# Optimization experiments

Measured on AMD Instinct MI355X. Metric: run time of the kernel, lower is better.

Reference implementation:

```python
import jax, jax.numpy as jnp
import numpy as np

NODES = 14      # input_size: nodes per graph
IN_F = 24       # seq_len: node feature dim
HID1 = 32
HID2 = 64       # hid_feats
HEADS = 2
OUT = 24        # output_size
B = 2048        # number of graphs
SLOPE = 0.2


def _make_edges():
    # fully connected (no self loops) within each 14-node graph
    pairs = np.array([(i, j) for i in range(NODES) for j in range(NODES) if i != j]).T  # [2,182]
    offs = (np.arange(B) * NODES)[:, None]
    src = (pairs[0][None, :] + offs).reshape(-1)
    dst = (pairs[1][None, :] + offs).reshape(-1)
    return np.stack([src, dst]).astype(np.int32)  # [2, 372736]


def setup_inputs() -> dict:
    key = jax.random.key(0)
    ks = jax.random.split(key, 16)
    N = B * NODES
    x = jax.random.normal(ks[0], (N, IN_F), dtype=jnp.float32)
    y = jax.random.normal(ks[1], (N, OUT), dtype=jnp.float32)
    edge_index = jnp.asarray(_make_edges())
    batch = jnp.repeat(jnp.arange(B, dtype=jnp.int32), NODES)
    s = 0.1
    params = dict(
        W1=jax.random.normal(ks[2], (IN_F, HEADS * HID1), dtype=jnp.float32) * s,
        a_src1=jax.random.normal(ks[3], (HEADS, HID1), dtype=jnp.float32) * s,
        a_dst1=jax.random.normal(ks[4], (HEADS, HID1), dtype=jnp.float32) * s,
        b1=jnp.zeros((HID1,), dtype=jnp.float32),
        W2=jax.random.normal(ks[5], (HID1, HEADS * HID2), dtype=jnp.float32) * s,
        a_src2=jax.random.normal(ks[6], (HEADS, HID2), dtype=jnp.float32) * s,
        a_dst2=jax.random.normal(ks[7], (HEADS, HID2), dtype=jnp.float32) * s,
        b2=jnp.zeros((HID2,), dtype=jnp.float32),
        Wf1=jax.random.normal(ks[8], (NODES, HID2, 8), dtype=jnp.float32) * s,
        bf1=jnp.zeros((NODES, 8), dtype=jnp.float32),
        Wf2=jax.random.normal(ks[9], (NODES, 8, OUT), dtype=jnp.float32) * s,
        bf2=jnp.zeros((NODES, OUT), dtype=jnp.float32),
    )
    return {"x": x, "y": y, "edge_index": edge_index, "batch": batch, **params}


def gat_conv(x, src, dst, W, a_src, a_dst, b):
    # PyG GATConv, concat=False (mean over heads), self-loops already in src/dst
    N = x.shape[0]
    H, F = a_src.shape
    xh = (x @ W).reshape(N, H, F)                       # [N,H,F]
    al_s = (xh * a_src).sum(-1)                         # [N,H]
    al_d = (xh * a_dst).sum(-1)                         # [N,H]
    alpha = jax.nn.leaky_relu(al_s[src] + al_d[dst], SLOPE)  # [E,H]
    amax = jax.ops.segment_max(alpha, dst, num_segments=N)
    ex = jnp.exp(alpha - amax[dst])
    den = jax.ops.segment_sum(ex, dst, num_segments=N)
    w = ex / den[dst]                                   # softmax per target node
    out = jax.ops.segment_sum(w[:, :, None] * xh[src], dst, num_segments=N)  # [N,H,F]
    return out.mean(axis=1) + b


def reference(x, y, edge_index, batch, W1, a_src1, a_dst1, b1, W2, a_src2, a_dst2, b2, Wf1, bf1, Wf2, bf2):
    N = x.shape[0]
    loops = jnp.arange(N, dtype=edge_index.dtype)
    src = jnp.concatenate([edge_index[0], loops])
    dst = jnp.concatenate([edge_index[1], loops])
    h = jax.nn.elu(gat_conv(x, src, dst, W1, a_src1, a_dst1, b1))   # [N,32]
    h = gat_conv(h, src, dst, W2, a_src2, a_dst2, b2)               # [N,64]
    # batch regroup: batch ids are contiguous per graph, so the Python
    # gather-loop in the original is exactly a reshape
    nb = N // NODES
    xg = h.reshape(nb, NODES, HID2).transpose(1, 0, 2)   # [14, B, 64]
    yg = y.reshape(nb, NODES, OUT)                       # [B, 14, out]
    # per-node-index MLP ensemble, batched over the 14 indices
    hh = jax.nn.relu(jnp.einsum('kbh,kho->kbo', xg, Wf1) + bf1[:, None, :])
    pred = jax.nn.sigmoid(jnp.einsum('kbo,kop->kbp', hh, Wf2) + bf2[:, None, :])  # [14,B,out]
    return pred, yg
```

## Files before the change

### kernel.cpp

```cpp
#include <hip/hip_runtime.h>

#define NODES 14
#define IN_F 24
#define HID1 32
#define HID2 64
#define OUT_F 24
#define SLOPE 0.2f

#define U_US1 0
#define U_UD1 48
#define U_US2 96
#define U_UD2 160

#define GPB 4
#define H1_S 36
#define H2_S 68
#define WT_S 20
#define PHASE_FENCE() __builtin_amdgcn_sched_barrier(0)

__global__ __launch_bounds__(256) void compute_uvecs(
    const float* __restrict__ W1, const float* __restrict__ a_src1,
    const float* __restrict__ a_dst1,
    const float* __restrict__ W2, const float* __restrict__ a_src2,
    const float* __restrict__ a_dst2, float* __restrict__ u)
{
  const int tid = threadIdx.x;
  if (tid < 96) {
    const int sd = (tid >= 48), r = tid - sd * 48;
    const int h = (r >= IN_F), k = r - h * IN_F;
    const float* av = sd ? a_dst1 : a_src1;
    float s = 0.f;
#pragma unroll
    for (int f = 0; f < HID1; ++f)
      s += W1[k * 64 + h * HID1 + f] * av[h * HID1 + f];
    u[(sd ? U_UD1 : U_US1) + h * IN_F + k] = s;
  } else if (tid < 224) {
    const int j = tid - 96;
    const int sd = (j >= 64), r = j - sd * 64;
    const int h = (r >= HID1), k = r - h * HID1;
    const float* av = sd ? a_dst2 : a_src2;
    float s = 0.f;
#pragma unroll
    for (int f = 0; f < HID2; ++f)
      s += W2[k * 128 + h * HID2 + f] * av[h * HID2 + f];
    u[(sd ? U_UD2 : U_US2) + h * HID1 + k] = s;
  }
}

__global__ __launch_bounds__(64 * GPB) void gnn_fused(
    const float* __restrict__ x, const float* __restrict__ y,
    const float* __restrict__ W1, const float* __restrict__ b1,
    const float* __restrict__ W2, const float* __restrict__ b2,
    const float* __restrict__ Wf1, const float* __restrict__ bf1,
    const float* __restrict__ Wf2, const float* __restrict__ bf2,
    const float* __restrict__ uvec,
    float* __restrict__ out, int ngraphs)
{
  const int tid  = threadIdx.x;
  const int lane = tid & 63;
  const int wv   = tid >> 6;
  const int gu   = __builtin_amdgcn_readfirstlane(blockIdx.x * GPB + wv);
  if (gu >= ngraphs) return;

  __shared__ __align__(16) float h1s[GPB][NODES * H1_S];
  __shared__ __align__(16) float h2s[GPB][NODES * H2_S];
  __shared__ __align__(16) float wt[GPB][28 * WT_S];
  __shared__ __align__(16) float als[GPB][32];
  __shared__ __align__(16) float ald[GPB][32];
  __shared__ __align__(16) float hhs[GPB][112];

  const float* xg = x + (size_t)gu * (NODES * IN_F);

  float w1r[IN_F];
#pragma unroll
  for (int k = 0; k < IN_F; ++k) w1r[k] = W1[k * 64 + lane];
  float w2r[64];
#pragma unroll
  for (int k = 0; k < HID1; ++k) {
    w2r[k]      = W2[k * 128 + lane];
    w2r[32 + k] = W2[k * 128 + 64 + lane];
  }
  PHASE_FENCE();

  {
    const float4* y4 = (const float4*)(y + (size_t)gu * (NODES * OUT_F));
    float4* o4 = (float4*)(out + (size_t)NODES * ngraphs * OUT_F
                               + (size_t)gu * (NODES * OUT_F));
    for (int i = lane; i < (NODES * OUT_F) / 4; i += 64) o4[i] = y4[i];
  }

  float xcol[NODES];
#pragma unroll 2
  for (int n = 0; n < NODES; ++n) {
    float acc = 0.f;
#pragma unroll
    for (int k = 0; k < IN_F; ++k) acc += xg[n * IN_F + k] * w1r[k];
    xcol[n] = acc;
  }

  if (lane < 56) {
    const int n = lane >> 2, h = (lane >> 1) & 1, sd = lane & 1;
    const float* uu = uvec + (sd ? U_UD1 : U_US1) + h * IN_F;
    float s = 0.f;
#pragma unroll
    for (int k4 = 0; k4 < 6; ++k4) {
      const float4 xv = *(const float4*)&xg[n * IN_F + k4 * 4];
      const float4 uv = *(const float4*)&uu[k4 * 4];
      s += xv.x * uv.x + xv.y * uv.y + xv.z * uv.z + xv.w * uv.w;
    }
    (sd ? ald : als)[wv][h * 16 + n] = s;
  }
  if (lane < NODES * 2) {
    const int j = lane >> 1, h = lane & 1;
    const float ad = ald[wv][h * 16 + j];
    const float4 A0 = *(const float4*)&als[wv][h * 16 + 0];
    const float4 A1 = *(const float4*)&als[wv][h * 16 + 4];
    const float4 A2 = *(const float4*)&als[wv][h * 16 + 8];
    const float2 A3 = *(const float2*)&als[wv][h * 16 + 12];
    float a[NODES] = {A0.x, A0.y, A0.z, A0.w, A1.x, A1.y, A1.z, A1.w,
                      A2.x, A2.y, A2.z, A2.w, A3.x, A3.y};
    float m = -1e30f;
#pragma unroll
    for (int i = 0; i < NODES; ++i) {
      float v = a[i] + ad;
      v = v > 0.f ? v : SLOPE * v;
      a[i] = v; m = fmaxf(m, v);
    }
    float den = 0.f;
#pragma unroll
    for (int i = 0; i < NODES; ++i) { a[i] = __expf(a[i] - m); den += a[i]; }
    const float r = 1.f / den;
    float* wr = &wt[wv][(j * 2 + h) * WT_S];
    *(float4*)&wr[0]  = make_float4(a[0]*r,  a[1]*r,  a[2]*r,  a[3]*r);
    *(float4*)&wr[4]  = make_float4(a[4]*r,  a[5]*r,  a[6]*r,  a[7]*r);
    *(float4*)&wr[8]  = make_float4(a[8]*r,  a[9]*r,  a[10]*r, a[11]*r);
    *(float2*)&wr[12] = make_float2(a[12]*r, a[13]*r);
  }

  {
    const int h = lane >> 5, f5 = lane & 31;
    const float bb = b1[f5];
#pragma unroll 2
    for (int n = 0; n < NODES; ++n) {
      const float* wr = &wt[wv][(n * 2 + h) * WT_S];
      const float4 w0 = *(const float4*)&wr[0];
      const float4 w1 = *(const float4*)&wr[4];
      const float4 w2 = *(const float4*)&wr[8];
      const float2 w3 = *(const float2*)&wr[12];
      float o = w0.x*xcol[0] + w0.y*xcol[1] + w0.z*xcol[2] + w0.w*xcol[3]
              + w1.x*xcol[4] + w1.y*xcol[5] + w1.z*xcol[6] + w1.w*xcol[7]
              + w2.x*xcol[8] + w2.y*xcol[9] + w2.z*xcol[10] + w2.w*xcol[11]
              + w3.x*xcol[12] + w3.y*xcol[13];
      const float oo = __shfl_xor(o, 32);
      if (h == 0) {
        const float v = 0.5f * (o + oo) + bb;
        h1s[wv][n * H1_S + f5] = v > 0.f ? v : expm1f(v);
      }
    }
  }
  PHASE_FENCE();

  float acc0[NODES], acc1[NODES];
#pragma unroll 2
  for (int n = 0; n < NODES; ++n) {
    const float4 v0 = *(const float4*)&h1s[wv][n * H1_S + 0];
    const float4 v1 = *(const float4*)&h1s[wv][n * H1_S + 4];
    const float4 v2 = *(const float4*)&h1s[wv][n * H1_S + 8];
    const float4 v3 = *(const float4*)&h1s[wv][n * H1_S + 12];
    const float4 v4 = *(const float4*)&h1s[wv][n * H1_S + 16];
    const float4 v5 = *(const float4*)&h1s[wv][n * H1_S + 20];
    const float4 v6 = *(const float4*)&h1s[wv][n * H1_S + 24];
    const float4 v7 = *(const float4*)&h1s[wv][n * H1_S + 28];
    acc0[n] = v0.x*w2r[0] + v0.y*w2r[1] + v0.z*w2r[2] + v0.w*w2r[3]
            + v1.x*w2r[4] + v1.y*w2r[5] + v1.z*w2r[6] + v1.w*w2r[7]
            + v2.x*w2r[8] + v2.y*w2r[9] + v2.z*w2r[10] + v2.w*w2r[11]
            + v3.x*w2r[12] + v3.y*w2r[13] + v3.z*w2r[14] + v3.w*w2r[15]
            + v4.x*w2r[16] + v4.y*w2r[17] + v4.z*w2r[18] + v4.w*w2r[19]
            + v5.x*w2r[20] + v5.y*w2r[21] + v5.z*w2r[22] + v5.w*w2r[23]
            + v6.x*w2r[24] + v6.y*w2r[25] + v6.z*w2r[26] + v6.w*w2r[27]
            + v7.x*w2r[28] + v7.y*w2r[29] + v7.z*w2r[30] + v7.w*w2r[31];
    acc1[n] = v0.x*w2r[32] + v0.y*w2r[33] + v0.z*w2r[34] + v0.w*w2r[35]
            + v1.x*w2r[36] + v1.y*w2r[37] + v1.z*w2r[38] + v1.w*w2r[39]
            + v2.x*w2r[40] + v2.y*w2r[41] + v2.z*w2r[42] + v2.w*w2r[43]
            + v3.x*w2r[44] + v3.y*w2r[45] + v3.z*w2r[46] + v3.w*w2r[47]
            + v4.x*w2r[48] + v4.y*w2r[49] + v4.z*w2r[50] + v4.w*w2r[51]
            + v5.x*w2r[52] + v5.y*w2r[53] + v5.z*w2r[54] + v5.w*w2r[55]
            + v6.x*w2r[56] + v6.y*w2r[57] + v6.z*w2r[58] + v6.w*w2r[59]
            + v7.x*w2r[60] + v7.y*w2r[61] + v7.z*w2r[62] + v7.w*w2r[63];
  }

  if (lane < 56) {
    const int n = lane >> 2, h = (lane >> 1) & 1, sd = lane & 1;
    const float* uu = uvec + (sd ? U_UD2 : U_US2) + h * HID1;
    float s = 0.f;
#pragma unroll
    for (int k4 = 0; k4 < 8; ++k4) {
      const float4 hv = *(const float4*)&h1s[wv][n * H1_S + k4 * 4];
      const float4 uv = *(const float4*)&uu[k4 * 4];
      s += hv.x * uv.x + hv.y * uv.y + hv.z * uv.z + hv.w * uv.w;
    }
    (sd ? ald : als)[wv][h * 16 + n] = s;
  }
  if (lane < NODES * 2) {
    const int j = lane >> 1, h = lane & 1;
    const float ad = ald[wv][h * 16 + j];
    const float4 A0 = *(const float4*)&als[wv][h * 16 + 0];
    const float4 A1 = *(const float4*)&als[wv][h * 16 + 4];
    const float4 A2 = *(const float4*)&als[wv][h * 16 + 8];
    const float2 A3 = *(const float2*)&als[wv][h * 16 + 12];
    float a[NODES] = {A0.x, A0.y, A0.z, A0.w, A1.x, A1.y, A1.z, A1.w,
                      A2.x, A2.y, A2.z, A2.w, A3.x, A3.y};
    float m = -1e30f;
#pragma unroll
    for (int i = 0; i < NODES; ++i) {
      float v = a[i] + ad;
      v = v > 0.f ? v : SLOPE * v;
      a[i] = v; m = fmaxf(m, v);
    }
    float den = 0.f;
#pragma unroll
    for (int i = 0; i < NODES; ++i) { a[i] = __expf(a[i] - m); den += a[i]; }
    const float r = 1.f / den;
    float* wr = &wt[wv][(j * 2 + h) * WT_S];
    *(float4*)&wr[0]  = make_float4(a[0]*r,  a[1]*r,  a[2]*r,  a[3]*r);
    *(float4*)&wr[4]  = make_float4(a[4]*r,  a[5]*r,  a[6]*r,  a[7]*r);
    *(float4*)&wr[8]  = make_float4(a[8]*r,  a[9]*r,  a[10]*r, a[11]*r);
    *(float2*)&wr[12] = make_float2(a[12]*r, a[13]*r);
  }

  {
    const float bb = b2[lane];
#pragma unroll 2
    for (int n = 0; n < NODES; ++n) {
      const float* wr0 = &wt[wv][(n * 2 + 0) * WT_S];
      const float* wr1 = &wt[wv][(n * 2 + 1) * WT_S];
      const float4 p0 = *(const float4*)&wr0[0];
      const float4 p1 = *(const float4*)&wr0[4];
      const float4 p2 = *(const float4*)&wr0[8];
      const float2 p3 = *(const float2*)&wr0[12];
      const float4 q0 = *(const float4*)&wr1[0];
      const float4 q1 = *(const float4*)&wr1[4];
      const float4 q2 = *(const float4*)&wr1[8];
      const float2 q3 = *(const float2*)&wr1[12];
      const float o0 = p0.x*acc0[0] + p0.y*acc0[1] + p0.z*acc0[2] + p0.w*acc0[3]
                     + p1.x*acc0[4] + p1.y*acc0[5] + p1.z*acc0[6] + p1.w*acc0[7]
                     + p2.x*acc0[8] + p2.y*acc0[9] + p2.z*acc0[10] + p2.w*acc0[11]
                     + p3.x*acc0[12] + p3.y*acc0[13];
      const float o1 = q0.x*acc1[0] + q0.y*acc1[1] + q0.z*acc1[2] + q0.w*acc1[3]
                     + q1.x*acc1[4] + q1.y*acc1[5] + q1.z*acc1[6] + q1.w*acc1[7]
                     + q2.x*acc1[8] + q2.y*acc1[9] + q2.z*acc1[10] + q2.w*acc1[11]
                     + q3.x*acc1[12] + q3.y*acc1[13];
      h2s[wv][n * H2_S + lane] = 0.5f * (o0 + o1) + bb;
    }
  }
  PHASE_FENCE();

  for (int idx = lane; idx < NODES * 8; idx += 64) {
    const int k = idx >> 3, e = idx & 7;
    float acc = bf1[k * 8 + e];
#pragma unroll
    for (int f4 = 0; f4 < 16; ++f4) {
      const float4 hv = *(const float4*)&h2s[wv][k * H2_S + f4 * 4];
      acc += hv.x * Wf1[(k * HID2 + f4 * 4 + 0) * 8 + e]
           + hv.y * Wf1[(k * HID2 + f4 * 4 + 1) * 8 + e]
           + hv.z * Wf1[(k * HID2 + f4 * 4 + 2) * 8 + e]
           + hv.w * Wf1[(k * HID2 + f4 * 4 + 3) * 8 + e];
    }
    hhs[wv][idx] = fmaxf(acc, 0.f);
  }

  for (int idx = lane; idx < NODES * OUT_F; idx += 64) {
    const int k = idx / OUT_F, o = idx - k * OUT_F;
    const float4 h0 = *(const float4*)&hhs[wv][k * 8];
    const float4 h1 = *(const float4*)&hhs[wv][k * 8 + 4];
    float acc = bf2[k * OUT_F + o]
              + h0.x * Wf2[(k * 8 + 0) * OUT_F + o]
              + h0.y * Wf2[(k * 8 + 1) * OUT_F + o]
              + h0.z * Wf2[(k * 8 + 2) * OUT_F + o]
              + h0.w * Wf2[(k * 8 + 3) * OUT_F + o]
              + h1.x * Wf2[(k * 8 + 4) * OUT_F + o]
              + h1.y * Wf2[(k * 8 + 5) * OUT_F + o]
              + h1.z * Wf2[(k * 8 + 6) * OUT_F + o]
              + h1.w * Wf2[(k * 8 + 7) * OUT_F + o];
    out[(size_t)k * ngraphs * OUT_F + (size_t)gu * OUT_F + o] =
        1.f / (1.f + __expf(-acc));
  }
}

extern "C" void kernel_launch(void* const* d_in, const int* in_sizes, int n_in,
                              void* d_out, int out_size, void* d_ws, size_t ws_size,
                              hipStream_t stream) {
  const float* x      = (const float*)d_in[0];
  const float* y      = (const float*)d_in[1];
  const float* W1     = (const float*)d_in[4];
  const float* a_src1 = (const float*)d_in[5];
  const float* a_dst1 = (const float*)d_in[6];
  const float* b1     = (const float*)d_in[7];
  const float* W2     = (const float*)d_in[8];
  const float* a_src2 = (const float*)d_in[9];
  const float* a_dst2 = (const float*)d_in[10];
  const float* b2     = (const float*)d_in[11];
  const float* Wf1    = (const float*)d_in[12];
  const float* bf1    = (const float*)d_in[13];
  const float* Wf2    = (const float*)d_in[14];
  const float* bf2    = (const float*)d_in[15];
  float* out = (float*)d_out;
  float* u   = (float*)d_ws;

  const int nnodes  = in_sizes[0] / IN_F;
  const int ngraphs = nnodes / NODES;
  const int nblocks = (ngraphs + GPB - 1) / GPB;

  hipLaunchKernelGGL(compute_uvecs, dim3(1), dim3(256), 0, stream,
                     W1, a_src1, a_dst1, W2, a_src2, a_dst2, u);
  hipLaunchKernelGGL(gnn_fused, dim3(nblocks), dim3(64 * GPB), 0, stream,
                     x, y, W1, b1, W2, b2, Wf1, bf1, Wf2, bf2, u, out, ngraphs);
}
```

Measured before the change: 30.52 us.

## Stage node features in LDS and vectorize final MLP loads and stores

The graph's x tile is copied into a padded shared-memory buffer with float4 loads, so the per-lane W1 projection and the attention-logit dot products read LDS instead of issuing scalar global loads. The first MLP layer now gives each lane two outputs and reads Wf1 as float2. The second layer gives each lane four outputs, using float4 loads of Wf2 and bf2 and a float4 store of the sigmoid results. This cuts global load instruction count and uses wider stores, at the cost of extra LDS space per block.

```diff
diff --git a/kernel.cpp b/kernel.cpp
--- a/kernel.cpp
+++ b/kernel.cpp
@@ -13,6 +13,7 @@
 #define U_UD2 160
 
 #define GPB 4
+#define XS_S 28
 #define H1_S 36
 #define H2_S 68
 #define WT_S 20
@@ -62,12 +63,13 @@
   const int gu   = __builtin_amdgcn_readfirstlane(blockIdx.x * GPB + wv);
   if (gu >= ngraphs) return;
 
+  __shared__ __align__(16) float xs[GPB][NODES * XS_S];
   __shared__ __align__(16) float h1s[GPB][NODES * H1_S];
   __shared__ __align__(16) float h2s[GPB][NODES * H2_S];
   __shared__ __align__(16) float wt[GPB][28 * WT_S];
   __shared__ __align__(16) float als[GPB][32];
   __shared__ __align__(16) float ald[GPB][32];
-  __shared__ __align__(16) float hhs[GPB][112];
+  __shared__ __align__(16) float hhs[GPB][120];
 
   const float* xg = x + (size_t)gu * (NODES * IN_F);
 
@@ -79,6 +81,15 @@
   for (int k = 0; k < HID1; ++k) {
     w2r[k]      = W2[k * 128 + lane];
     w2r[32 + k] = W2[k * 128 + 64 + lane];
+  }
+  {
+    const float4* x4 = (const float4*)xg;
+#pragma unroll
+    for (int i = lane; i < (NODES * IN_F) / 4; i += 64) {
+      const float4 v = x4[i];
+      const int n = (i * 4) / IN_F, k = (i * 4) - n * IN_F;
+      *(float4*)&xs[wv][n * XS_S + k] = v;
+    }
   }
   PHASE_FENCE();
 
@@ -94,7 +105,11 @@
   for (int n = 0; n < NODES; ++n) {
     float acc = 0.f;
 #pragma unroll
-    for (int k = 0; k < IN_F; ++k) acc += xg[n * IN_F + k] * w1r[k];
+    for (int k4 = 0; k4 < IN_F / 4; ++k4) {
+      const float4 xv = *(const float4*)&xs[wv][n * XS_S + k4 * 4];
+      acc += xv.x * w1r[k4 * 4 + 0] + xv.y * w1r[k4 * 4 + 1]
+           + xv.z * w1r[k4 * 4 + 2] + xv.w * w1r[k4 * 4 + 3];
+    }
     xcol[n] = acc;
   }
 
@@ -104,7 +119,7 @@
     float s = 0.f;
 #pragma unroll
     for (int k4 = 0; k4 < 6; ++k4) {
-      const float4 xv = *(const float4*)&xg[n * IN_F + k4 * 4];
+      const float4 xv = *(const float4*)&xs[wv][n * XS_S + k4 * 4];
       const float4 uv = *(const float4*)&uu[k4 * 4];
       s += xv.x * uv.x + xv.y * uv.y + xv.z * uv.z + xv.w * uv.w;
     }
@@ -255,35 +270,40 @@
   }
   PHASE_FENCE();
 
-  for (int idx = lane; idx < NODES * 8; idx += 64) {
-    const int k = idx >> 3, e = idx & 7;
-    float acc = bf1[k * 8 + e];
+  if (lane < 56) {
+    const int k = lane >> 2, e2 = (lane & 3) * 2;
+    float a0 = bf1[k * 8 + e2], a1 = bf1[k * 8 + e2 + 1];
 #pragma unroll
     for (int f4 = 0; f4 < 16; ++f4) {
       const float4 hv = *(const float4*)&h2s[wv][k * H2_S + f4 * 4];
-      acc += hv.x * Wf1[(k * HID2 + f4 * 4 + 0) * 8 + e]
-           + hv.y * Wf1[(k * HID2 + f4 * 4 + 1) * 8 + e]
-           + hv.z * Wf1[(k * HID2 + f4 * 4 + 2) * 8 + e]
-           + hv.w * Wf1[(k * HID2 + f4 * 4 + 3) * 8 + e];
-    }
-    hhs[wv][idx] = fmaxf(acc, 0.f);
-  }
-
-  for (int idx = lane; idx < NODES * OUT_F; idx += 64) {
-    const int k = idx / OUT_F, o = idx - k * OUT_F;
+      const float2 wa = *(const float2*)&Wf1[(k * HID2 + f4 * 4 + 0) * 8 + e2];
+      const float2 wb = *(const float2*)&Wf1[(k * HID2 + f4 * 4 + 1) * 8 + e2];
+      const float2 wc = *(const float2*)&Wf1[(k * HID2 + f4 * 4 + 2) * 8 + e2];
+      const float2 wd = *(const float2*)&Wf1[(k * HID2 + f4 * 4 + 3) * 8 + e2];
+      a0 += hv.x * wa.x + hv.y * wb.x + hv.z * wc.x + hv.w * wd.x;
+      a1 += hv.x * wa.y + hv.y * wb.y + hv.z * wc.y + hv.w * wd.y;
+    }
+    *(float2*)&hhs[wv][k * 8 + e2] =
+        make_float2(fmaxf(a0, 0.f), fmaxf(a1, 0.f));
+  }
+
+  for (int idx = lane; idx < NODES * (OUT_F / 4); idx += 64) {
+    const int k = idx / (OUT_F / 4), o4 = (idx - k * (OUT_F / 4)) * 4;
     const float4 h0 = *(const float4*)&hhs[wv][k * 8];
     const float4 h1 = *(const float4*)&hhs[wv][k * 8 + 4];
-    float acc = bf2[k * OUT_F + o]
-              + h0.x * Wf2[(k * 8 + 0) * OUT_F + o]
-              + h0.y * Wf2[(k * 8 + 1) * OUT_F + o]
-              + h0.z * Wf2[(k * 8 + 2) * OUT_F + o]
-              + h0.w * Wf2[(k * 8 + 3) * OUT_F + o]
-              + h1.x * Wf2[(k * 8 + 4) * OUT_F + o]
-              + h1.y * Wf2[(k * 8 + 5) * OUT_F + o]
-              + h1.z * Wf2[(k * 8 + 6) * OUT_F + o]
-              + h1.w * Wf2[(k * 8 + 7) * OUT_F + o];
-    out[(size_t)k * ngraphs * OUT_F + (size_t)gu * OUT_F + o] =
-        1.f / (1.f + __expf(-acc));
+    float4 acc = *(const float4*)&bf2[k * OUT_F + o4];
+    const float he[8] = {h0.x, h0.y, h0.z, h0.w, h1.x, h1.y, h1.z, h1.w};
+#pragma unroll
+    for (int e = 0; e < 8; ++e) {
+      const float4 wv4 = *(const float4*)&Wf2[(k * 8 + e) * OUT_F + o4];
+      acc.x += he[e] * wv4.x; acc.y += he[e] * wv4.y;
+      acc.z += he[e] * wv4.z; acc.w += he[e] * wv4.w;
+    }
+    acc.x = 1.f / (1.f + __expf(-acc.x));
+    acc.y = 1.f / (1.f + __expf(-acc.y));
+    acc.z = 1.f / (1.f + __expf(-acc.z));
+    acc.w = 1.f / (1.f + __expf(-acc.w));
+    *(float4*)&out[(size_t)k * ngraphs * OUT_F + (size_t)gu * OUT_F + o4] = acc;
   }
 }
 
```

Result: no change. 30.53 us (+0.0%).
